# Kernel tuning notes

Hardware: AMD Instinct MI355X
Metric: run time of the kernel (lower is better)

The kernel has to match this reference:

```python
import jax, jax.numpy as jnp
import numpy as np

D = 1024      # model dim
DH = 64       # dim_head
H = 8         # heads
INNER = DH * H
L = 6         # depth
NL = 64       # num_latents
MF = 128      # max_num_frames
FF = 4 * D    # ff_mult * dim
B, T, F, V = 4, 8, 4, 256


def _ln(x, g, b):
    m = x.mean(-1, keepdims=True)
    v = x.var(-1, keepdims=True)
    return (x - m) / jnp.sqrt(v + 1e-5) * g + b


def setup_inputs() -> dict:
    key = jax.random.key(0)
    ks = jax.random.split(key, 8)
    s = 0.02
    x = jax.random.normal(ks[0], (B, T, F, V, D), jnp.float32)
    latents = jax.random.normal(ks[1], (NL, D), jnp.float32)
    frame_embs = jax.random.normal(ks[2], (MF, D), jnp.float32)
    Wq = jax.random.normal(ks[3], (L, D, INNER), jnp.float32) * s
    Wkv = jax.random.normal(ks[4], (L, D, 2 * INNER), jnp.float32) * s
    Wo = jax.random.normal(ks[5], (L, INNER, D), jnp.float32) * s
    W1 = jax.random.normal(ks[6], (L, D, FF), jnp.float32) * s
    W2 = jax.random.normal(ks[7], (L, FF, D), jnp.float32) * s
    ones = jnp.ones((L, D), jnp.float32)
    zeros = jnp.zeros((L, D), jnp.float32)
    return dict(
        x=x, latents=latents, frame_embs=frame_embs,
        g_media=ones, b_media=zeros, g_lat=ones, b_lat=zeros,
        Wq=Wq, Wkv=Wkv, Wo=Wo, g_ff=ones, b_ff=zeros, W1=W1, W2=W2,
        g_out=jnp.ones((D,), jnp.float32), b_out=jnp.zeros((D,), jnp.float32),
    )


def reference(x, latents, frame_embs, g_media, b_media, g_lat, b_lat,
              Wq, Wkv, Wo, g_ff, b_ff, W1, W2, g_out, b_out):
    scale = DH ** -0.5
    # add frame embeddings (indexed by T, as in original code), merge F,v dims
    x = x + frame_embs[:T][None, :, None, None, :]
    x = x.reshape(B, T, F * V, D)
    lat0 = jnp.broadcast_to(latents, (B, T, NL, D))

    def split_heads(a):  # (b, t, n, h*d) -> (b, h, t, n, d)
        return a.reshape(B, T, -1, H, DH).transpose(0, 3, 1, 2, 4)

    def block(lat, p):
        gm, bm, gl, bl, wq, wkv, wo, gf, bf, w1, w2 = p
        xm = _ln(x, gm, bm)
        ln_l = _ln(lat, gl, bl)
        q = (ln_l @ wq) * scale
        kv = jnp.concatenate([xm, ln_l], axis=-2) @ wkv
        k, v = jnp.split(kv, 2, axis=-1)
        q, k, v = split_heads(q), split_heads(k), split_heads(v)
        sim = jnp.einsum('bhtid,bhtjd->bhtij', q, k)
        attn = jax.nn.softmax(sim, axis=-1)
        o = jnp.einsum('bhtij,bhtjd->bhtid', attn, v)
        o = o.transpose(0, 2, 3, 1, 4).reshape(B, T, NL, INNER)
        lat = o @ wo + lat
        ff = jax.nn.gelu(_ln(lat, gf, bf) @ w1, approximate=False) @ w2
        return lat + ff, None

    lat, _ = jax.lax.scan(block, lat0,
                          (g_media, b_media, g_lat, b_lat, Wq, Wkv, Wo,
                           g_ff, b_ff, W1, W2))
    return _ln(lat, g_out, b_out)
```

## Files before the change

### kernel.cpp

```cpp
#include <hip/hip_runtime.h>
#include <math.h>

#define D_      1024
#define DH_     64
#define H_      8
#define INNER_  512
#define L_      6
#define NL_     64
#define FF_     4096
#define B_      4
#define T_      8
#define FV_     1024
#define BT_     32
#define MROWS_  32768
#define NKV_    1088
#define KVROWS_ 34816
#define ZB_     256

typedef __bf16 bf16;
typedef __bf16 bf16x8 __attribute__((ext_vector_type(8)));
typedef __bf16 bf16x4 __attribute__((ext_vector_type(4)));
typedef float  f32x4  __attribute__((ext_vector_type(4)));

#define BARRIER() { asm volatile("" ::: "memory"); __builtin_amdgcn_s_barrier(); asm volatile("" ::: "memory"); }

__device__ __forceinline__ void gload_lds16(const bf16* g, bf16* l) {
    __builtin_amdgcn_global_load_lds(
        (const __attribute__((address_space(1))) unsigned int*)g,
        (__attribute__((address_space(3))) unsigned int*)l, 16, 0, 0);
}

__device__ __forceinline__ float wred_sum(float v) {
#pragma unroll
    for (int o = 32; o > 0; o >>= 1) v += __shfl_xor(v, o, 64);
    return v;
}

__device__ __forceinline__ float gelu_f(float x) {
    return 0.5f * x * (1.0f + erff(x * 0.70710678118654752440f));
}

__global__ __launch_bounds__(256) void xhat_k(const float* __restrict__ x,
                                              const float* __restrict__ fe,
                                              bf16* __restrict__ xhat) {
    __shared__ float red[8];
    int row = blockIdx.x;
    int t = (row >> 10) & 7;
    const float* xr = x + (size_t)row * D_;
    const float* fr_ = fe + (size_t)t * D_;
    int tid = threadIdx.x, c = tid * 4;
    float4 v = *(const float4*)(xr + c);
    float4 f = *(const float4*)(fr_ + c);
    v.x += f.x; v.y += f.y; v.z += f.z; v.w += f.w;
    float s = v.x + v.y + v.z + v.w;
    float ss = v.x * v.x + v.y * v.y + v.z * v.z + v.w * v.w;
    s = wred_sum(s); ss = wred_sum(ss);
    if ((tid & 63) == 0) { red[tid >> 6] = s; red[4 + (tid >> 6)] = ss; }
    __syncthreads();
    s = red[0] + red[1] + red[2] + red[3];
    ss = red[4] + red[5] + red[6] + red[7];
    float mean = s * (1.0f / D_);
    float rstd = rsqrtf(ss * (1.0f / D_) - mean * mean + 1e-5f);
    bf16x4 o;
    o[0] = (bf16)((v.x - mean) * rstd);
    o[1] = (bf16)((v.y - mean) * rstd);
    o[2] = (bf16)((v.z - mean) * rstd);
    o[3] = (bf16)((v.w - mean) * rstd);
    *(bf16x4*)(xhat + (size_t)row * D_ + c) = o;
}

__global__ __launch_bounds__(256) void latinit_k(const float* __restrict__ latents,
                                                 float* __restrict__ lat) {
    int row = blockIdx.x;
    int i = row & 63;
    int c = threadIdx.x * 4;
    float4 v = *(const float4*)(latents + (size_t)i * D_ + c);
    *(float4*)(lat + (size_t)row * D_ + c) = v;
}

template<int OUTF>
__global__ __launch_bounds__(256) void ln_k(const float* __restrict__ in,
                                            const float* __restrict__ g,
                                            const float* __restrict__ b,
                                            void* __restrict__ out) {
    __shared__ float red[8];
    int row = blockIdx.x;
    const float* x = in + (size_t)row * D_;
    int tid = threadIdx.x, c = tid * 4;
    float4 v = *(const float4*)(x + c);
    float s = v.x + v.y + v.z + v.w;
    float ss = v.x * v.x + v.y * v.y + v.z * v.z + v.w * v.w;
    s = wred_sum(s); ss = wred_sum(ss);
    if ((tid & 63) == 0) { red[tid >> 6] = s; red[4 + (tid >> 6)] = ss; }
    __syncthreads();
    s = red[0] + red[1] + red[2] + red[3];
    ss = red[4] + red[5] + red[6] + red[7];
    float mean = s * (1.0f / D_);
    float rstd = rsqrtf(ss * (1.0f / D_) - mean * mean + 1e-5f);
    float4 gv = *(const float4*)(g + c);
    float4 bv = *(const float4*)(b + c);
    float o0 = (v.x - mean) * rstd * gv.x + bv.x;
    float o1 = (v.y - mean) * rstd * gv.y + bv.y;
    float o2 = (v.z - mean) * rstd * gv.z + bv.z;
    float o3 = (v.w - mean) * rstd * gv.w + bv.w;
    if (OUTF) {
        *(float4*)((float*)out + (size_t)row * D_ + c) = make_float4(o0, o1, o2, o3);
    } else {
        bf16x4 o; o[0] = (bf16)o0; o[1] = (bf16)o1; o[2] = (bf16)o2; o[3] = (bf16)o3;
        *(bf16x4*)((bf16*)out + (size_t)row * D_ + c) = o;
    }
}

template<int NP, int OUTF>
__global__ __launch_bounds__(256) void accln_k(float* __restrict__ lat,
                                               const float* __restrict__ p, long long s,
                                               const float* __restrict__ g,
                                               const float* __restrict__ b,
                                               void* __restrict__ out) {
    __shared__ float red[8];
    int row = blockIdx.x;
    int tid = threadIdx.x, c = tid * 4;
    float* lr = lat + (size_t)row * D_;
    float4 a = *(const float4*)(lr + c);
#pragma unroll
    for (int w = 0; w < NP; w++) {
        float4 x = *(const float4*)(p + (size_t)w * s + (size_t)row * D_ + c);
        a.x += x.x; a.y += x.y; a.z += x.z; a.w += x.w;
    }
    if (!OUTF) *(float4*)(lr + c) = a;
    float sm = a.x + a.y + a.z + a.w;
    float ss = a.x * a.x + a.y * a.y + a.z * a.z + a.w * a.w;
    sm = wred_sum(sm); ss = wred_sum(ss);
    if ((tid & 63) == 0) { red[tid >> 6] = sm; red[4 + (tid >> 6)] = ss; }
    __syncthreads();
    sm = red[0] + red[1] + red[2] + red[3];
    ss = red[4] + red[5] + red[6] + red[7];
    float mean = sm * (1.0f / D_);
    float rstd = rsqrtf(ss * (1.0f / D_) - mean * mean + 1e-5f);
    float4 gv = *(const float4*)(g + c);
    float4 bv = *(const float4*)(b + c);
    float o0 = (a.x - mean) * rstd * gv.x + bv.x;
    float o1 = (a.y - mean) * rstd * gv.y + bv.y;
    float o2 = (a.z - mean) * rstd * gv.z + bv.z;
    float o3 = (a.w - mean) * rstd * gv.w + bv.w;
    if (OUTF) {
        *(float4*)((float*)out + (size_t)row * D_ + c) = make_float4(o0, o1, o2, o3);
    } else {
        bf16x4 o; o[0] = (bf16)o0; o[1] = (bf16)o1; o[2] = (bf16)o2; o[3] = (bf16)o3;
        *(bf16x4*)((bf16*)out + (size_t)row * D_ + c) = o;
    }
}

__device__ __forceinline__ void wt_tile(const float* __restrict__ in, int R, int C,
                                        bf16* __restrict__ out, int bx, int by,
                                        const float* __restrict__ sc) {
    __shared__ float t[32][33];
    int c0 = bx * 32, r0 = by * 32;
    int tx = threadIdx.x & 31, ty = threadIdx.x >> 5;
#pragma unroll
    for (int i = 0; i < 4; i++)
        t[ty + i * 8][tx] = in[(size_t)(r0 + ty + i * 8) * C + c0 + tx];
    __syncthreads();
    float scale = sc ? sc[r0 + tx] : 1.0f;
#pragma unroll
    for (int i = 0; i < 4; i++)
        out[(size_t)(c0 + ty + i * 8) * R + r0 + tx] = (bf16)(t[tx][ty + i * 8] * scale);
}

__global__ __launch_bounds__(256) void wprep_k(const float* __restrict__ wq,
                                               const float* __restrict__ wkv,
                                               const float* __restrict__ wo,
                                               const float* __restrict__ w1,
                                               const float* __restrict__ w2,
                                               const float* __restrict__ gm,
                                               bf16* __restrict__ BcatQ,
                                               bf16* __restrict__ BcatKV,
                                               bf16* __restrict__ WkvTg,
                                               bf16* __restrict__ WoT,
                                               bf16* __restrict__ W1T,
                                               bf16* __restrict__ W2T) {
    int id = blockIdx.x;
    if (id < 512)            wt_tile(wq, D_, INNER_, BcatQ, id & 15, id >> 4, nullptr);
    else if (id < 1536)  { int i = id - 512;  wt_tile(wkv, D_, 2 * INNER_, BcatKV, i & 31, i >> 5, nullptr); }
    else if (id < 2560)  { int i = id - 1536; wt_tile(wkv, D_, 2 * INNER_, WkvTg, i & 31, i >> 5, gm); }
    else if (id < 3072)  { int i = id - 2560; wt_tile(wo, INNER_, D_, WoT, i & 31, i >> 5, nullptr); }
    else if (id < 7168)  { int i = id - 3072; wt_tile(w1, D_, FF_, W1T, i & 127, i >> 7, nullptr); }
    else                 { int i = id - 7168; wt_tile(w2, FF_, D_, W2T, i & 31, i >> 5, nullptr); }
}

__global__ __launch_bounds__(256) void bias_k(const float* __restrict__ bm,
                                              const float* __restrict__ wkv,
                                              float* __restrict__ bkv) {
    int n = blockIdx.x * 256 + threadIdx.x;
    float s = 0.0f;
    for (int k = 0; k < D_; k++) s += bm[k] * wkv[(size_t)k * (2 * INNER_) + n];
    bkv[n] = s;
}

__global__ __launch_bounds__(512, 1) void gemm_kv(const bf16* __restrict__ Ag,
                                                  const bf16* __restrict__ Bg,
                                                  bf16* __restrict__ KVb,
                                                  bf16* __restrict__ vt,
                                                  const float* __restrict__ bias) {
    __shared__ bf16 lds[2][32768];
    const int lda = D_, ldb = D_;
    const int tid = threadIdx.x;
    const int w = tid >> 6, lane = tid & 63;
    const int wm = w >> 2, wn = w & 3;
    const size_t m0 = (size_t)blockIdx.x * 256;
    const size_t n0 = (size_t)blockIdx.y * 256;
    const int nt = 16;

    const int p0 = (w * 2) * 64 + lane, p1 = p0 + 64;
    const int sr0 = p0 >> 3, sk0 = ((p0 & 7) ^ (sr0 & 7)) * 8;
    const int sr1 = p1 >> 3, sk1 = ((p1 & 7) ^ (sr1 & 7)) * 8;
    const int scw0 = (w * 2) * 512, scw1 = scw0 + 512;

    auto STAGE = [&](const bf16* g, int ld, size_t row0, int k0, bf16* bufb, int rb) {
        gload_lds16(g + (row0 + sr0) * (size_t)ld + k0 + sk0, bufb + rb + scw0);
        gload_lds16(g + (row0 + sr1) * (size_t)ld + k0 + sk1, bufb + rb + scw1);
    };

    const int fr = lane & 15;
    const int pK0 = (((lane >> 4)) ^ (fr & 7)) * 8;
    const int pK1 = ((4 + (lane >> 4)) ^ (fr & 7)) * 8;
    const size_t aoff = (size_t)(wm * 128 + fr) * 64;
    const size_t boff = 16384 + (size_t)(wn * 64 + fr) * 64;

    f32x4 acc[8][4];
#pragma unroll
    for (int i = 0; i < 8; i++)
#pragma unroll
        for (int j = 0; j < 4; j++)
#pragma unroll
            for (int r = 0; r < 4; r++) acc[i][j][r] = 0.0f;

    STAGE(Bg, ldb, n0,       0, lds[0], 16384);
    STAGE(Bg, ldb, n0 + 128, 0, lds[0], 24576);
    STAGE(Ag, lda, m0,       0, lds[0], 0);
    STAGE(Ag, lda, m0 + 128, 0, lds[0], 8192);
    STAGE(Bg, ldb, n0,       64, lds[1], 16384);
    STAGE(Bg, ldb, n0 + 128, 64, lds[1], 24576);
    STAGE(Ag, lda, m0,       64, lds[1], 0);
    asm volatile("s_waitcnt vmcnt(6)");
    BARRIER();

    for (int t = 0; t < nt; ++t) {
        const bf16* lb = lds[t & 1];
        bf16* lbw = lds[t & 1];
        bf16* lbn = lds[(t + 1) & 1];
        const int kt1 = (t + 1) << 6, kt2 = (t + 2) << 6;
        bf16x8 bfr[4][2];

        {
#pragma unroll
            for (int j = 0; j < 4; j++) {
                bfr[j][0] = *(const bf16x8*)(lb + boff + j * 1024 + pK0);
                bfr[j][1] = *(const bf16x8*)(lb + boff + j * 1024 + pK1);
            }
            bf16x8 a00 = *(const bf16x8*)(lb + aoff + 0 * 1024 + pK0);
            bf16x8 a01 = *(const bf16x8*)(lb + aoff + 0 * 1024 + pK1);
            bf16x8 a10 = *(const bf16x8*)(lb + aoff + 1 * 1024 + pK0);
            bf16x8 a11 = *(const bf16x8*)(lb + aoff + 1 * 1024 + pK1);
            if (t + 1 < nt) STAGE(Ag, lda, m0 + 128, kt1, lbn, 8192);
            BARRIER();
            asm volatile("s_waitcnt lgkmcnt(0)");
            __builtin_amdgcn_s_setprio(1);
#pragma unroll
            for (int j = 0; j < 4; j++) {
                acc[0][j] = __builtin_amdgcn_mfma_f32_16x16x32_bf16(a00, bfr[j][0], acc[0][j], 0, 0, 0);
                acc[0][j] = __builtin_amdgcn_mfma_f32_16x16x32_bf16(a01, bfr[j][1], acc[0][j], 0, 0, 0);
                acc[1][j] = __builtin_amdgcn_mfma_f32_16x16x32_bf16(a10, bfr[j][0], acc[1][j], 0, 0, 0);
                acc[1][j] = __builtin_amdgcn_mfma_f32_16x16x32_bf16(a11, bfr[j][1], acc[1][j], 0, 0, 0);
            }
            __builtin_amdgcn_s_setprio(0);
            BARRIER();
        }
        {
            bf16x8 a00 = *(const bf16x8*)(lb + aoff + 2 * 1024 + pK0);
            bf16x8 a01 = *(const bf16x8*)(lb + aoff + 2 * 1024 + pK1);
            bf16x8 a10 = *(const bf16x8*)(lb + aoff + 3 * 1024 + pK0);
            bf16x8 a11 = *(const bf16x8*)(lb + aoff + 3 * 1024 + pK1);
            if (t + 2 < nt) STAGE(Bg, ldb, n0, kt2, lbw, 16384);
            BARRIER();
            asm volatile("s_waitcnt lgkmcnt(0)");
            __builtin_amdgcn_s_setprio(1);
#pragma unroll
            for (int j = 0; j < 4; j++) {
                acc[2][j] = __builtin_amdgcn_mfma_f32_16x16x32_bf16(a00, bfr[j][0], acc[2][j], 0, 0, 0);
                acc[2][j] = __builtin_amdgcn_mfma_f32_16x16x32_bf16(a01, bfr[j][1], acc[2][j], 0, 0, 0);
                acc[3][j] = __builtin_amdgcn_mfma_f32_16x16x32_bf16(a10, bfr[j][0], acc[3][j], 0, 0, 0);
                acc[3][j] = __builtin_amdgcn_mfma_f32_16x16x32_bf16(a11, bfr[j][1], acc[3][j], 0, 0, 0);
            }
            __builtin_amdgcn_s_setprio(0);
            BARRIER();
        }
        {
            bf16x8 a00 = *(const bf16x8*)(lb + aoff + 4 * 1024 + pK0);
            bf16x8 a01 = *(const bf16x8*)(lb + aoff + 4 * 1024 + pK1);
            bf16x8 a10 = *(const bf16x8*)(lb + aoff + 5 * 1024 + pK0);
            bf16x8 a11 = *(const bf16x8*)(lb + aoff + 5 * 1024 + pK1);
            if (t + 2 < nt) STAGE(Bg, ldb, n0 + 128, kt2, lbw, 24576);
            BARRIER();
            asm volatile("s_waitcnt lgkmcnt(0)");
            __builtin_amdgcn_s_setprio(1);
#pragma unroll
            for (int j = 0; j < 4; j++) {
                acc[4][j] = __builtin_amdgcn_mfma_f32_16x16x32_bf16(a00, bfr[j][0], acc[4][j], 0, 0, 0);
                acc[4][j] = __builtin_amdgcn_mfma_f32_16x16x32_bf16(a01, bfr[j][1], acc[4][j], 0, 0, 0);
                acc[5][j] = __builtin_amdgcn_mfma_f32_16x16x32_bf16(a10, bfr[j][0], acc[5][j], 0, 0, 0);
                acc[5][j] = __builtin_amdgcn_mfma_f32_16x16x32_bf16(a11, bfr[j][1], acc[5][j], 0, 0, 0);
            }
            __builtin_amdgcn_s_setprio(0);
            BARRIER();
        }
        {
            bf16x8 a00 = *(const bf16x8*)(lb + aoff + 6 * 1024 + pK0);
            bf16x8 a01 = *(const bf16x8*)(lb + aoff + 6 * 1024 + pK1);
            bf16x8 a10 = *(const bf16x8*)(lb + aoff + 7 * 1024 + pK0);
            bf16x8 a11 = *(const bf16x8*)(lb + aoff + 7 * 1024 + pK1);
            if (t + 2 < nt) STAGE(Ag, lda, m0, kt2, lbw, 0);
            BARRIER();
            asm volatile("s_waitcnt lgkmcnt(0)");
            __builtin_amdgcn_s_setprio(1);
#pragma unroll
            for (int j = 0; j < 4; j++) {
                acc[6][j] = __builtin_amdgcn_mfma_f32_16x16x32_bf16(a00, bfr[j][0], acc[6][j], 0, 0, 0);
                acc[6][j] = __builtin_amdgcn_mfma_f32_16x16x32_bf16(a01, bfr[j][1], acc[6][j], 0, 0, 0);
                acc[7][j] = __builtin_amdgcn_mfma_f32_16x16x32_bf16(a10, bfr[j][0], acc[7][j], 0, 0, 0);
                acc[7][j] = __builtin_amdgcn_mfma_f32_16x16x32_bf16(a11, bfr[j][1], acc[7][j], 0, 0, 0);
            }
            __builtin_amdgcn_s_setprio(0);
            if (t < nt - 2)       { asm volatile("s_waitcnt vmcnt(6)"); }
            else if (t == nt - 2) { asm volatile("s_waitcnt vmcnt(0)"); }
            BARRIER();
        }
    }

    const int fq = (lane >> 4) * 4;
#pragma unroll
    for (int i = 0; i < 8; i++)
#pragma unroll
        for (int j = 0; j < 4; j++) {
            size_t cb = n0 + wn * 64 + j * 16 + fr;
            float bv = bias[cb];
            size_t mb = m0 + wm * 128 + i * 16 + fq;
            if (cb < 512) {
#pragma unroll
                for (int r = 0; r < 4; r++) {
                    size_t m = mb + r;
                    size_t rb = m + ((m >> 10) << 6);
                    KVb[rb * 512 + cb] = (bf16)(acc[i][j][r] + bv);
                }
            } else {
                int hh = ((int)cb - 512) >> 6, dh = ((int)cb - 512) & 63;
                size_t bt = mb >> 10, jl = mb & 1023;
                bf16x4 v4;
#pragma unroll
                for (int r = 0; r < 4; r++) v4[r] = (bf16)(acc[i][j][r] + bv);
                *(bf16x4*)(vt + ((bt * 8 + hh) * 64 + dh) * (size_t)NKV_ + jl) = v4;
            }
        }
}

template<int MODE, int CMAP>
__global__ __launch_bounds__(256) void gemm128(const bf16* __restrict__ A, int lda,
                                               const bf16* __restrict__ Bw, int ldb,
                                               void* __restrict__ C, int ldc,
                                               int K, float scale,
                                               long long czs, void* __restrict__ C2,
                                               void* __restrict__ C3) {
    __shared__ bf16 As[128 * 32];
    __shared__ bf16 Bs[128 * 32];
    const int tid = threadIdx.x;
    const int wave = tid >> 6;
    const int lane = tid & 63;
    const size_t m0 = (size_t)blockIdx.x * 128;
    const size_t n0 = (size_t)blockIdx.y * 128;
    const int wm = (wave >> 1) * 64;
    const int wn = (wave & 1) * 64;

    const int klen = K / gridDim.z;
    const int koff = blockIdx.z * klen;

    const int r0 = tid >> 2;
    const int c0 = ((tid & 3) ^ ((tid >> 3) & 3)) * 8;
    const bf16* ga0 = A + (m0 + r0) * lda + c0 + koff;
    const bf16* ga1 = A + (m0 + r0 + 64) * lda + c0 + koff;
    const bf16* gb0 = Bw + (n0 + r0) * ldb + c0 + koff;
    const bf16* gb1 = Bw + (n0 + r0 + 64) * ldb + c0 + koff;
    bf16* la0 = As + wave * 512;
    bf16* la1 = As + 2048 + wave * 512;
    bf16* lb0 = Bs + wave * 512;
    bf16* lb1 = Bs + 2048 + wave * 512;

    f32x4 acc[4][4];
#pragma unroll
    for (int i = 0; i < 4; i++)
#pragma unroll
        for (int j = 0; j < 4; j++)
#pragma unroll
            for (int r = 0; r < 4; r++) acc[i][j][r] = 0.0f;

    const int fr = lane & 15;
    const int q = lane >> 4;
    const int sw = (q ^ ((fr >> 1) & 3)) * 8;

    for (int kt = 0; kt < klen; kt += 32) {
        gload_lds16(ga0 + kt, la0);
        gload_lds16(ga1 + kt, la1);
        gload_lds16(gb0 + kt, lb0);
        gload_lds16(gb1 + kt, lb1);
        __syncthreads();
        bf16x8 af[4], bfv[4];
#pragma unroll
        for (int i = 0; i < 4; i++) {
            af[i]  = *(const bf16x8*)(As + (wm + i * 16 + fr) * 32 + sw);
            bfv[i] = *(const bf16x8*)(Bs + (wn + i * 16 + fr) * 32 + sw);
        }
#pragma unroll
        for (int i = 0; i < 4; i++)
#pragma unroll
            for (int j = 0; j < 4; j++)
                acc[i][j] = __builtin_amdgcn_mfma_f32_16x16x32_bf16(af[i], bfv[j], acc[i][j], 0, 0, 0);
        __syncthreads();
    }

    const int fq = (lane >> 4) * 4;
#pragma unroll
    for (int i = 0; i < 4; i++)
#pragma unroll
        for (int j = 0; j < 4; j++) {
            size_t cb = n0 + wn + j * 16 + fr;
            size_t mb = m0 + wm + i * 16 + fq;
            if (CMAP == 3) {
                if (cb < 512) {
#pragma unroll
                    for (int r = 0; r < 4; r++)
                        ((bf16*)C)[(mb + r) * 512 + cb] = (bf16)(acc[i][j][r] * scale);
                } else if (cb < 1024) {
#pragma unroll
                    for (int r = 0; r < 4; r++) {
                        size_t m = mb + r;
                        size_t rb = (m >> 6) * (size_t)NKV_ + 1024 + (m & 63);
                        ((bf16*)C2)[rb * 512 + (cb - 512)] = (bf16)acc[i][j][r];
                    }
                } else {
                    int hh = ((int)cb - 1024) >> 6, dh = ((int)cb - 1024) & 63;
                    size_t bt = mb >> 6, jl = 1024 + (mb & 63);
                    bf16x4 v4;
#pragma unroll
                    for (int r = 0; r < 4; r++) v4[r] = (bf16)acc[i][j][r];
                    *(bf16x4*)((bf16*)C3 + ((bt * 8 + hh) * 64 + dh) * (size_t)NKV_ + jl) = v4;
                }
            } else {
#pragma unroll
                for (int r = 0; r < 4; r++) {
                    float v = acc[i][j][r];
                    if (MODE == 4) {
                        ((float*)C + blockIdx.z * czs)[(mb + r) * ldc + cb] = v;
                    } else {
                        if (MODE == 3) v = gelu_f(v);
                        ((bf16*)C)[(mb + r) * ldc + cb] = (bf16)v;
                    }
                }
            }
        }
}

__global__ __launch_bounds__(256, 2) void attn_k(const bf16* __restrict__ qb,
                                                 const bf16* __restrict__ KVb,
                                                 const bf16* __restrict__ vt,
                                                 bf16* __restrict__ ob) {
    __shared__ float comb[4][64 * 66];
    __shared__ float sc[4][64];
    __shared__ float mw[4][64], lw[4][64];
    const int z = blockIdx.x, bt = z >> 3, h = z & 7;
    const int tid = threadIdx.x, w = tid >> 6, lane = tid & 63;
    const int fr = lane & 15, g = lane >> 4;
    const bf16* Qz = qb + (size_t)(bt * 64) * INNER_ + h * DH_;
    const bf16* Kz = KVb + (size_t)bt * NKV_ * 512 + h * DH_;
    const bf16* Vz = vt + (size_t)z * (DH_ * NKV_);
    bf16* Pw = (bf16*)(&comb[w][0]);

    bf16x8 qf[4][2];
#pragma unroll
    for (int nj = 0; nj < 4; nj++)
#pragma unroll
        for (int ks = 0; ks < 2; ks++)
            qf[nj][ks] = *(const bf16x8*)(Qz + (size_t)(fr + 16 * nj) * INNER_ + g * 8 + ks * 32);

    f32x4 acc_o[4][4];
#pragma unroll
    for (int i = 0; i < 4; i++)
#pragma unroll
        for (int j = 0; j < 4; j++)
#pragma unroll
            for (int r = 0; r < 4; r++) acc_o[i][j][r] = 0.0f;
    float m_reg[4] = {-INFINITY, -INFINITY, -INFINITY, -INFINITY};
    float l_reg[4] = {0.0f, 0.0f, 0.0f, 0.0f};

    const int nch = (w == 0) ? 5 : 4;
    for (int ci = 0; ci < nch; ci++) {
        const int kc0 = (w + ci * 4) * 64;
        f32x4 s[4][4];
#pragma unroll
        for (int i = 0; i < 4; i++)
#pragma unroll
            for (int j = 0; j < 4; j++)
#pragma unroll
                for (int r = 0; r < 4; r++) s[i][j][r] = 0.0f;
#pragma unroll
        for (int ks = 0; ks < 2; ks++) {
            bf16x8 kf[4];
#pragma unroll
            for (int mi = 0; mi < 4; mi++)
                kf[mi] = *(const bf16x8*)(Kz + (size_t)(kc0 + fr + 16 * mi) * 512 + g * 8 + ks * 32);
#pragma unroll
            for (int mi = 0; mi < 4; mi++)
#pragma unroll
                for (int nj = 0; nj < 4; nj++)
                    s[mi][nj] = __builtin_amdgcn_mfma_f32_16x16x32_bf16(kf[mi], qf[nj][ks], s[mi][nj], 0, 0, 0);
        }
        float pmax[4];
#pragma unroll
        for (int nj = 0; nj < 4; nj++) {
            float mx = s[0][nj][0];
#pragma unroll
            for (int mi = 0; mi < 4; mi++)
#pragma unroll
                for (int r = 0; r < 4; r++) mx = fmaxf(mx, s[mi][nj][r]);
            mx = fmaxf(mx, __shfl_xor(mx, 16, 64));
            mx = fmaxf(mx, __shfl_xor(mx, 32, 64));
            pmax[nj] = mx;
        }
        bool grew = (pmax[0] > m_reg[0]) || (pmax[1] > m_reg[1]) ||
                    (pmax[2] > m_reg[2]) || (pmax[3] > m_reg[3]);
        if (__any(grew ? 1 : 0)) {
            float so[4];
#pragma unroll
            for (int nj = 0; nj < 4; nj++) {
                float mn = fmaxf(m_reg[nj], pmax[nj]);
                so[nj] = __expf(m_reg[nj] - mn);
                m_reg[nj] = mn;
                l_reg[nj] *= so[nj];
            }
            if (g == 0) {
#pragma unroll
                for (int nj = 0; nj < 4; nj++) sc[w][fr + 16 * nj] = so[nj];
            }
            asm volatile("s_waitcnt lgkmcnt(0)" ::: "memory");
#pragma unroll
            for (int mi = 0; mi < 4; mi++)
#pragma unroll
                for (int r = 0; r < 4; r++) {
                    float sq = sc[w][16 * mi + 4 * g + r];
#pragma unroll
                    for (int jd = 0; jd < 4; jd++) acc_o[mi][jd][r] *= sq;
                }
        }
        float psum[4] = {0.0f, 0.0f, 0.0f, 0.0f};
#pragma unroll
        for (int mi = 0; mi < 4; mi++)
#pragma unroll
            for (int nj = 0; nj < 4; nj++) {
                bf16x4 pb4;
#pragma unroll
                for (int r = 0; r < 4; r++) {
                    float pv = __expf(s[mi][nj][r] - m_reg[nj]);
                    psum[nj] += pv;
                    pb4[r] = (bf16)pv;
                }
                *(bf16x4*)(Pw + (size_t)(fr + 16 * nj) * 72 + 16 * mi + 4 * g) = pb4;
            }
#pragma unroll
        for (int nj = 0; nj < 4; nj++) {
            float ps = psum[nj];
            ps += __shfl_xor(ps, 16, 64);
            ps += __shfl_xor(ps, 32, 64);
            l_reg[nj] += ps;
        }
        asm volatile("s_waitcnt lgkmcnt(0)" ::: "memory");
#pragma unroll
        for (int ks = 0; ks < 2; ks++) {
            bf16x8 af[4], vf[4];
#pragma unroll
            for (int mi = 0; mi < 4; mi++)
                af[mi] = *(const bf16x8*)(Pw + (size_t)(fr + 16 * mi) * 72 + g * 8 + ks * 32);
#pragma unroll
            for (int jd = 0; jd < 4; jd++)
                vf[jd] = *(const bf16x8*)(Vz + (size_t)(fr + 16 * jd) * NKV_ + kc0 + g * 8 + ks * 32);
#pragma unroll
            for (int mi = 0; mi < 4; mi++)
#pragma unroll
                for (int jd = 0; jd < 4; jd++)
                    acc_o[mi][jd] = __builtin_amdgcn_mfma_f32_16x16x32_bf16(af[mi], vf[jd], acc_o[mi][jd], 0, 0, 0);
        }
    }

    if (g == 0) {
#pragma unroll
        for (int nj = 0; nj < 4; nj++) {
            mw[w][fr + 16 * nj] = m_reg[nj];
            lw[w][fr + 16 * nj] = l_reg[nj];
        }
    }
    asm volatile("s_waitcnt lgkmcnt(0)" ::: "memory");
#pragma unroll
    for (int mi = 0; mi < 4; mi++)
#pragma unroll
        for (int jd = 0; jd < 4; jd++)
#pragma unroll
            for (int r = 0; r < 4; r++)
                comb[w][(16 * mi + 4 * g + r) * 66 + fr + 16 * jd] = acc_o[mi][jd][r];
    __syncthreads();
    {
        int q = tid >> 2, d0 = (tid & 3) * 16;
        float M = fmaxf(fmaxf(mw[0][q], mw[1][q]), fmaxf(mw[2][q], mw[3][q]));
        float al[4], l = 0.0f;
#pragma unroll
        for (int ww = 0; ww < 4; ww++) { al[ww] = __expf(mw[ww][q] - M); l += al[ww] * lw[ww][q]; }
        float inv = 1.0f / l;
        bf16 outv[16];
#pragma unroll
        for (int dd = 0; dd < 16; dd++) {
            float o = 0.0f;
#pragma unroll
            for (int ww = 0; ww < 4; ww++) o += comb[ww][q * 66 + d0 + dd] * al[ww];
            outv[dd] = (bf16)(o * inv);
        }
        bf16* dst = ob + (size_t)(bt * 64 + q) * INNER_ + h * 64 + d0;
        *(bf16x8*)dst = *(bf16x8*)outv;
        *(bf16x8*)(dst + 8) = *(bf16x8*)(outv + 8);
    }
}

extern "C" void kernel_launch(void* const* d_in, const int* in_sizes, int n_in,
                              void* d_out, int out_size, void* d_ws, size_t ws_size,
                              hipStream_t stream) {
    const float* x       = (const float*)d_in[0];
    const float* latents = (const float*)d_in[1];
    const float* fe      = (const float*)d_in[2];
    const float* g_media = (const float*)d_in[3];
    const float* b_media = (const float*)d_in[4];
    const float* g_lat   = (const float*)d_in[5];
    const float* b_lat   = (const float*)d_in[6];
    const float* Wq      = (const float*)d_in[7];
    const float* Wkv     = (const float*)d_in[8];
    const float* Wo      = (const float*)d_in[9];
    const float* g_ff    = (const float*)d_in[10];
    const float* b_ff    = (const float*)d_in[11];
    const float* W1      = (const float*)d_in[12];
    const float* W2      = (const float*)d_in[13];
    const float* g_out   = (const float*)d_in[14];
    const float* b_out   = (const float*)d_in[15];

    char* p = (char*)d_ws;
    auto alloc = [&](size_t bytes) { char* r = p; p += (bytes + 255) & ~(size_t)255; return r; };
    bf16*  xhat = (bf16*)alloc((size_t)MROWS_ * D_ * 2);
    float* lat  = (float*)alloc((size_t)2048 * D_ * 4);
    bf16*  lnl  = (bf16*)alloc((size_t)2048 * D_ * 2);
    bf16*  qb   = (bf16*)alloc((size_t)2048 * INNER_ * 2);
    bf16*  KVb  = (bf16*)alloc((size_t)KVROWS_ * 512 * 2);
    bf16*  vt   = (bf16*)alloc((size_t)ZB_ * DH_ * NKV_ * 2);
    bf16*  ob   = (bf16*)alloc((size_t)2048 * INNER_ * 2);
    bf16*  Bcat = (bf16*)alloc((size_t)1536 * D_ * 2);
    bf16*  WkvTg= (bf16*)alloc((size_t)D_ * D_ * 2);
    bf16*  WoT  = (bf16*)alloc((size_t)D_ * INNER_ * 2);
    bf16*  W1T  = (bf16*)alloc((size_t)FF_ * D_ * 2);
    bf16*  W2T  = (bf16*)alloc((size_t)D_ * FF_ * 2);
    float* bkv  = (float*)alloc(1024 * 4);
    float* ffp  = (float*)alloc((size_t)4 * 2048 * D_ * 4);
    bf16*  ffh  = vt;

    xhat_k<<<MROWS_, 256, 0, stream>>>(x, fe, xhat);
    latinit_k<<<2048, 256, 0, stream>>>(latents, lat);
    ln_k<0><<<2048, 256, 0, stream>>>(lat, g_lat, b_lat, lnl);

    const long long PS = (long long)2048 * D_;

    for (int l = 0; l < L_; l++) {
        const float* gm = g_media + (size_t)l * D_;
        const float* bm = b_media + (size_t)l * D_;
        const float* gf = g_ff + (size_t)l * D_;
        const float* bf_ = b_ff + (size_t)l * D_;
        const float* wq = Wq + (size_t)l * D_ * INNER_;
        const float* wkv = Wkv + (size_t)l * D_ * 2 * INNER_;
        const float* wo = Wo + (size_t)l * INNER_ * D_;
        const float* w1 = W1 + (size_t)l * D_ * FF_;
        const float* w2 = W2 + (size_t)l * FF_ * D_;

        wprep_k<<<11264, 256, 0, stream>>>(wq, wkv, wo, w1, w2, gm,
                                           Bcat, Bcat + (size_t)512 * D_, WkvTg, WoT, W1T, W2T);
        bias_k<<<4, 256, 0, stream>>>(bm, wkv, bkv);

        gemm_kv<<<dim3(128, 4), 512, 0, stream>>>(xhat, WkvTg, KVb, vt, bkv);
        gemm128<0, 3><<<dim3(16, 12), 256, 0, stream>>>(
            lnl, D_, Bcat, D_, qb, 0, D_, 0.125f, 0, KVb, vt);

        attn_k<<<ZB_, 256, 0, stream>>>(qb, KVb, vt, ob);

        gemm128<4, 0><<<dim3(16, 8, 2), 256, 0, stream>>>(
            ob, INNER_, WoT, INNER_, ffp, D_, INNER_, 1.0f, PS, nullptr, nullptr);
        accln_k<2, 0><<<2048, 256, 0, stream>>>(lat, ffp, PS, gf, bf_, lnl);

        gemm128<3, 0><<<dim3(16, 32), 256, 0, stream>>>(
            lnl, D_, W1T, D_, ffh, FF_, D_, 1.0f, 0, nullptr, nullptr);
        gemm128<4, 0><<<dim3(16, 8, 4), 256, 0, stream>>>(
            ffh, FF_, W2T, FF_, ffp, D_, FF_, 1.0f, PS, nullptr, nullptr);
        if (l < L_ - 1) {
            accln_k<4, 0><<<2048, 256, 0, stream>>>(lat, ffp, PS,
                g_lat + (size_t)(l + 1) * D_, b_lat + (size_t)(l + 1) * D_, lnl);
        } else {
            accln_k<4, 1><<<2048, 256, 0, stream>>>(lat, ffp, PS, g_out, b_out, (float*)d_out);
        }
    }
}
```

Baseline: 1.583 ms.

## Software-pipeline GEMM LDS fragment loads, add FF GEMM kernel, fuse bias into wprep

The KV GEMM main loop is restructured so the next A/B fragments are loaded from LDS while the current MFMAs run. The B fragments are double-buffered in registers across K tiles and the wait/barrier points are adjusted. A new 128x256-tile, 512-thread gemm_ff kernel with the same pipelining replaces gemm128 for the two feed-forward GEMMs, with GELU moved into its epilogue. The separate bias kernel is removed and the bias is computed inside the weight-transpose tiles via atomicAdd after a memset, which trades a serial loop for atomics and more register pressure.

```diff
diff --git a/kernel.cpp b/kernel.cpp
--- a/kernel.cpp
+++ b/kernel.cpp
@@ -23,6 +23,7 @@
 typedef float  f32x4  __attribute__((ext_vector_type(4)));
 
 #define BARRIER() { asm volatile("" ::: "memory"); __builtin_amdgcn_s_barrier(); asm volatile("" ::: "memory"); }
+#define ENDPH() { __builtin_amdgcn_sched_barrier(0); asm volatile("s_waitcnt lgkmcnt(0)"); __builtin_amdgcn_sched_barrier(0); BARRIER(); }
 
 __device__ __forceinline__ void gload_lds16(const bf16* g, bf16* l) {
     __builtin_amdgcn_global_load_lds(
@@ -153,7 +154,9 @@
 
 __device__ __forceinline__ void wt_tile(const float* __restrict__ in, int R, int C,
                                         bf16* __restrict__ out, int bx, int by,
-                                        const float* __restrict__ sc) {
+                                        const float* __restrict__ sc,
+                                        const float* __restrict__ bm,
+                                        float* __restrict__ bkv) {
     __shared__ float t[32][33];
     int c0 = bx * 32, r0 = by * 32;
     int tx = threadIdx.x & 31, ty = threadIdx.x >> 5;
@@ -165,6 +168,12 @@
 #pragma unroll
     for (int i = 0; i < 4; i++)
         out[(size_t)(c0 + ty + i * 8) * R + r0 + tx] = (bf16)(t[tx][ty + i * 8] * scale);
+    if (bm && ty == 0) {
+        float s = 0.0f;
+#pragma unroll
+        for (int r = 0; r < 32; r++) s += bm[r0 + r] * t[r][tx];
+        atomicAdd(&bkv[c0 + tx], s);
+    }
 }
 
 __global__ __launch_bounds__(256) void wprep_k(const float* __restrict__ wq,
@@ -173,6 +182,8 @@
                                                const float* __restrict__ w1,
                                                const float* __restrict__ w2,
                                                const float* __restrict__ gm,
+                                               const float* __restrict__ bm,
+                                               float* __restrict__ bkv,
                                                bf16* __restrict__ BcatQ,
                                                bf16* __restrict__ BcatKV,
                                                bf16* __restrict__ WkvTg,
@@ -180,21 +191,12 @@
                                                bf16* __restrict__ W1T,
                                                bf16* __restrict__ W2T) {
     int id = blockIdx.x;
-    if (id < 512)            wt_tile(wq, D_, INNER_, BcatQ, id & 15, id >> 4, nullptr);
-    else if (id < 1536)  { int i = id - 512;  wt_tile(wkv, D_, 2 * INNER_, BcatKV, i & 31, i >> 5, nullptr); }
-    else if (id < 2560)  { int i = id - 1536; wt_tile(wkv, D_, 2 * INNER_, WkvTg, i & 31, i >> 5, gm); }
-    else if (id < 3072)  { int i = id - 2560; wt_tile(wo, INNER_, D_, WoT, i & 31, i >> 5, nullptr); }
-    else if (id < 7168)  { int i = id - 3072; wt_tile(w1, D_, FF_, W1T, i & 127, i >> 7, nullptr); }
-    else                 { int i = id - 7168; wt_tile(w2, FF_, D_, W2T, i & 31, i >> 5, nullptr); }
-}
-
-__global__ __launch_bounds__(256) void bias_k(const float* __restrict__ bm,
-                                              const float* __restrict__ wkv,
-                                              float* __restrict__ bkv) {
-    int n = blockIdx.x * 256 + threadIdx.x;
-    float s = 0.0f;
-    for (int k = 0; k < D_; k++) s += bm[k] * wkv[(size_t)k * (2 * INNER_) + n];
-    bkv[n] = s;
+    if (id < 512)            wt_tile(wq, D_, INNER_, BcatQ, id & 15, id >> 4, nullptr, nullptr, nullptr);
+    else if (id < 1536)  { int i = id - 512;  wt_tile(wkv, D_, 2 * INNER_, BcatKV, i & 31, i >> 5, nullptr, nullptr, nullptr); }
+    else if (id < 2560)  { int i = id - 1536; wt_tile(wkv, D_, 2 * INNER_, WkvTg, i & 31, i >> 5, gm, bm, bkv); }
+    else if (id < 3072)  { int i = id - 2560; wt_tile(wo, INNER_, D_, WoT, i & 31, i >> 5, nullptr, nullptr, nullptr); }
+    else if (id < 7168)  { int i = id - 3072; wt_tile(w1, D_, FF_, W1T, i & 127, i >> 7, nullptr, nullptr, nullptr); }
+    else                 { int i = id - 7168; wt_tile(w2, FF_, D_, W2T, i & 31, i >> 5, nullptr, nullptr, nullptr); }
 }
 
 __global__ __launch_bounds__(512, 1) void gemm_kv(const bf16* __restrict__ Ag,
@@ -235,6 +237,33 @@
 #pragma unroll
             for (int r = 0; r < 4; r++) acc[i][j][r] = 0.0f;
 
+    bf16x8 aX[4], aY[4], bA[4][2], bB[4][2];
+
+    auto LDA2 = [&](const bf16* lb, int i0, bf16x8 (&d)[4]) {
+        d[0] = *(const bf16x8*)(lb + aoff + (size_t)i0 * 1024 + pK0);
+        d[1] = *(const bf16x8*)(lb + aoff + (size_t)i0 * 1024 + pK1);
+        d[2] = *(const bf16x8*)(lb + aoff + (size_t)(i0 + 1) * 1024 + pK0);
+        d[3] = *(const bf16x8*)(lb + aoff + (size_t)(i0 + 1) * 1024 + pK1);
+    };
+    auto LDB8 = [&](const bf16* lb, bf16x8 (&bb)[4][2]) {
+#pragma unroll
+        for (int j = 0; j < 4; j++) {
+            bb[j][0] = *(const bf16x8*)(lb + boff + j * 1024 + pK0);
+            bb[j][1] = *(const bf16x8*)(lb + boff + j * 1024 + pK1);
+        }
+    };
+    auto MM2 = [&](int i0, bf16x8 (&a)[4], bf16x8 (&bb)[4][2]) {
+        __builtin_amdgcn_s_setprio(1);
+#pragma unroll
+        for (int j = 0; j < 4; j++) {
+            acc[i0][j]     = __builtin_amdgcn_mfma_f32_16x16x32_bf16(a[0], bb[j][0], acc[i0][j], 0, 0, 0);
+            acc[i0][j]     = __builtin_amdgcn_mfma_f32_16x16x32_bf16(a[1], bb[j][1], acc[i0][j], 0, 0, 0);
+            acc[i0 + 1][j] = __builtin_amdgcn_mfma_f32_16x16x32_bf16(a[2], bb[j][0], acc[i0 + 1][j], 0, 0, 0);
+            acc[i0 + 1][j] = __builtin_amdgcn_mfma_f32_16x16x32_bf16(a[3], bb[j][1], acc[i0 + 1][j], 0, 0, 0);
+        }
+        __builtin_amdgcn_s_setprio(0);
+    };
+
     STAGE(Bg, ldb, n0,       0, lds[0], 16384);
     STAGE(Bg, ldb, n0 + 128, 0, lds[0], 24576);
     STAGE(Ag, lda, m0,       0, lds[0], 0);
@@ -244,97 +273,37 @@
     STAGE(Ag, lda, m0,       64, lds[1], 0);
     asm volatile("s_waitcnt vmcnt(6)");
     BARRIER();
-
-    for (int t = 0; t < nt; ++t) {
-        const bf16* lb = lds[t & 1];
-        bf16* lbw = lds[t & 1];
-        bf16* lbn = lds[(t + 1) & 1];
-        const int kt1 = (t + 1) << 6, kt2 = (t + 2) << 6;
-        bf16x8 bfr[4][2];
-
-        {
-#pragma unroll
-            for (int j = 0; j < 4; j++) {
-                bfr[j][0] = *(const bf16x8*)(lb + boff + j * 1024 + pK0);
-                bfr[j][1] = *(const bf16x8*)(lb + boff + j * 1024 + pK1);
-            }
-            bf16x8 a00 = *(const bf16x8*)(lb + aoff + 0 * 1024 + pK0);
-            bf16x8 a01 = *(const bf16x8*)(lb + aoff + 0 * 1024 + pK1);
-            bf16x8 a10 = *(const bf16x8*)(lb + aoff + 1 * 1024 + pK0);
-            bf16x8 a11 = *(const bf16x8*)(lb + aoff + 1 * 1024 + pK1);
-            if (t + 1 < nt) STAGE(Ag, lda, m0 + 128, kt1, lbn, 8192);
-            BARRIER();
-            asm volatile("s_waitcnt lgkmcnt(0)");
-            __builtin_amdgcn_s_setprio(1);
-#pragma unroll
-            for (int j = 0; j < 4; j++) {
-                acc[0][j] = __builtin_amdgcn_mfma_f32_16x16x32_bf16(a00, bfr[j][0], acc[0][j], 0, 0, 0);
-                acc[0][j] = __builtin_amdgcn_mfma_f32_16x16x32_bf16(a01, bfr[j][1], acc[0][j], 0, 0, 0);
-                acc[1][j] = __builtin_amdgcn_mfma_f32_16x16x32_bf16(a10, bfr[j][0], acc[1][j], 0, 0, 0);
-                acc[1][j] = __builtin_amdgcn_mfma_f32_16x16x32_bf16(a11, bfr[j][1], acc[1][j], 0, 0, 0);
-            }
-            __builtin_amdgcn_s_setprio(0);
-            BARRIER();
-        }
-        {
-            bf16x8 a00 = *(const bf16x8*)(lb + aoff + 2 * 1024 + pK0);
-            bf16x8 a01 = *(const bf16x8*)(lb + aoff + 2 * 1024 + pK1);
-            bf16x8 a10 = *(const bf16x8*)(lb + aoff + 3 * 1024 + pK0);
-            bf16x8 a11 = *(const bf16x8*)(lb + aoff + 3 * 1024 + pK1);
-            if (t + 2 < nt) STAGE(Bg, ldb, n0, kt2, lbw, 16384);
-            BARRIER();
-            asm volatile("s_waitcnt lgkmcnt(0)");
-            __builtin_amdgcn_s_setprio(1);
-#pragma unroll
-            for (int j = 0; j < 4; j++) {
-                acc[2][j] = __builtin_amdgcn_mfma_f32_16x16x32_bf16(a00, bfr[j][0], acc[2][j], 0, 0, 0);
-                acc[2][j] = __builtin_amdgcn_mfma_f32_16x16x32_bf16(a01, bfr[j][1], acc[2][j], 0, 0, 0);
-                acc[3][j] = __builtin_amdgcn_mfma_f32_16x16x32_bf16(a10, bfr[j][0], acc[3][j], 0, 0, 0);
-                acc[3][j] = __builtin_amdgcn_mfma_f32_16x16x32_bf16(a11, bfr[j][1], acc[3][j], 0, 0, 0);
-            }
-            __builtin_amdgcn_s_setprio(0);
-            BARRIER();
-        }
-        {
-            bf16x8 a00 = *(const bf16x8*)(lb + aoff + 4 * 1024 + pK0);
-            bf16x8 a01 = *(const bf16x8*)(lb + aoff + 4 * 1024 + pK1);
-            bf16x8 a10 = *(const bf16x8*)(lb + aoff + 5 * 1024 + pK0);
-            bf16x8 a11 = *(const bf16x8*)(lb + aoff + 5 * 1024 + pK1);
-            if (t + 2 < nt) STAGE(Bg, ldb, n0 + 128, kt2, lbw, 24576);
-            BARRIER();
-            asm volatile("s_waitcnt lgkmcnt(0)");
-            __builtin_amdgcn_s_setprio(1);
-#pragma unroll
-            for (int j = 0; j < 4; j++) {
-                acc[4][j] = __builtin_amdgcn_mfma_f32_16x16x32_bf16(a00, bfr[j][0], acc[4][j], 0, 0, 0);
-                acc[4][j] = __builtin_amdgcn_mfma_f32_16x16x32_bf16(a01, bfr[j][1], acc[4][j], 0, 0, 0);
-                acc[5][j] = __builtin_amdgcn_mfma_f32_16x16x32_bf16(a10, bfr[j][0], acc[5][j], 0, 0, 0);
-                acc[5][j] = __builtin_amdgcn_mfma_f32_16x16x32_bf16(a11, bfr[j][1], acc[5][j], 0, 0, 0);
-            }
-            __builtin_amdgcn_s_setprio(0);
-            BARRIER();
-        }
-        {
-            bf16x8 a00 = *(const bf16x8*)(lb + aoff + 6 * 1024 + pK0);
-            bf16x8 a01 = *(const bf16x8*)(lb + aoff + 6 * 1024 + pK1);
-            bf16x8 a10 = *(const bf16x8*)(lb + aoff + 7 * 1024 + pK0);
-            bf16x8 a11 = *(const bf16x8*)(lb + aoff + 7 * 1024 + pK1);
-            if (t + 2 < nt) STAGE(Ag, lda, m0, kt2, lbw, 0);
-            BARRIER();
-            asm volatile("s_waitcnt lgkmcnt(0)");
-            __builtin_amdgcn_s_setprio(1);
-#pragma unroll
-            for (int j = 0; j < 4; j++) {
-                acc[6][j] = __builtin_amdgcn_mfma_f32_16x16x32_bf16(a00, bfr[j][0], acc[6][j], 0, 0, 0);
-                acc[6][j] = __builtin_amdgcn_mfma_f32_16x16x32_bf16(a01, bfr[j][1], acc[6][j], 0, 0, 0);
-                acc[7][j] = __builtin_amdgcn_mfma_f32_16x16x32_bf16(a10, bfr[j][0], acc[7][j], 0, 0, 0);
-                acc[7][j] = __builtin_amdgcn_mfma_f32_16x16x32_bf16(a11, bfr[j][1], acc[7][j], 0, 0, 0);
-            }
-            __builtin_amdgcn_s_setprio(0);
-            if (t < nt - 2)       { asm volatile("s_waitcnt vmcnt(6)"); }
-            else if (t == nt - 2) { asm volatile("s_waitcnt vmcnt(0)"); }
-            BARRIER();
-        }
+    LDB8(lds[0], bA);
+    LDA2(lds[0], 0, aX);
+
+    auto tile4 = [&](const bf16* lb, bf16* lbn, bf16x8 (&BU)[4][2], bf16x8 (&BL)[4][2], int t) {
+        bf16* lbw = (bf16*)lb;
+        LDA2(lb, 2, aY);
+        if (t + 1 < nt) STAGE(Ag, lda, m0 + 128, (t + 1) << 6, lbn, 8192);
+        MM2(0, aX, BU);
+        ENDPH();
+        LDA2(lb, 4, aX);
+        if (t + 2 < nt) STAGE(Bg, ldb, n0, (t + 2) << 6, lbw, 16384);
+        MM2(2, aY, BU);
+        ENDPH();
+        LDA2(lb, 6, aY);
+        if (t + 2 < nt) STAGE(Bg, ldb, n0 + 128, (t + 2) << 6, lbw, 24576);
+        MM2(4, aX, BU);
+        __builtin_amdgcn_sched_barrier(0);
+        asm volatile("s_waitcnt lgkmcnt(0)");
+        __builtin_amdgcn_sched_barrier(0);
+        if (t < nt - 2)       { asm volatile("s_waitcnt vmcnt(4)"); }
+        else if (t == nt - 2) { asm volatile("s_waitcnt vmcnt(0)"); }
+        BARRIER();
+        if (t + 1 < nt) { LDB8(lbn, BL); LDA2(lbn, 0, aX); }
+        if (t + 2 < nt) STAGE(Ag, lda, m0, (t + 2) << 6, lbw, 0);
+        MM2(6, aY, BU);
+        ENDPH();
+    };
+
+    for (int t = 0; t < nt; t += 2) {
+        tile4(lds[0], lds[1], bA, bB, t);
+        tile4(lds[1], lds[0], bB, bA, t + 1);
     }
 
     const int fq = (lane >> 4) * 4;
@@ -359,6 +328,126 @@
 #pragma unroll
                 for (int r = 0; r < 4; r++) v4[r] = (bf16)(acc[i][j][r] + bv);
                 *(bf16x4*)(vt + ((bt * 8 + hh) * 64 + dh) * (size_t)NKV_ + jl) = v4;
+            }
+        }
+}
+
+template<int MODE>
+__global__ __launch_bounds__(512, 1) void gemm_ff(const bf16* __restrict__ Ag, int lda,
+                                                  const bf16* __restrict__ Bg, int ldb,
+                                                  void* __restrict__ C, int ldc,
+                                                  int K, long long czs) {
+    __shared__ bf16 lds[2][24576];
+    const int tid = threadIdx.x;
+    const int w = tid >> 6, lane = tid & 63;
+    const int wm = w >> 2, wn = w & 3;
+    const size_t m0 = (size_t)blockIdx.x * 128;
+    const size_t n0 = (size_t)blockIdx.y * 256;
+    const int klen = K / gridDim.z;
+    const int koff = blockIdx.z * klen;
+    const int nt = klen >> 6;
+
+    const int p0 = (w * 2) * 64 + lane, p1 = p0 + 64;
+    const int sr0 = p0 >> 3, sk0 = ((p0 & 7) ^ (sr0 & 7)) * 8;
+    const int sr1 = p1 >> 3, sk1 = ((p1 & 7) ^ (sr1 & 7)) * 8;
+    const int scw0 = (w * 2) * 512, scw1 = scw0 + 512;
+
+    auto STAGE = [&](const bf16* g, int ld, size_t row0, int k0, bf16* bufb, int rb) {
+        gload_lds16(g + (row0 + sr0) * (size_t)ld + k0 + sk0, bufb + rb + scw0);
+        gload_lds16(g + (row0 + sr1) * (size_t)ld + k0 + sk1, bufb + rb + scw1);
+    };
+
+    const int fr = lane & 15;
+    const int pK0 = (((lane >> 4)) ^ (fr & 7)) * 8;
+    const int pK1 = ((4 + (lane >> 4)) ^ (fr & 7)) * 8;
+    const size_t aoff = (size_t)(wm * 64 + fr) * 64;
+    const size_t boff = 8192 + (size_t)(wn * 64 + fr) * 64;
+
+    f32x4 acc[4][4];
+#pragma unroll
+    for (int i = 0; i < 4; i++)
+#pragma unroll
+        for (int j = 0; j < 4; j++)
+#pragma unroll
+            for (int r = 0; r < 4; r++) acc[i][j][r] = 0.0f;
+
+    bf16x8 aX[2], aY[2], bA[4][2], bB[4][2];
+
+    auto LDA1 = [&](const bf16* lb, int i0, bf16x8 (&d)[2]) {
+        d[0] = *(const bf16x8*)(lb + aoff + (size_t)i0 * 1024 + pK0);
+        d[1] = *(const bf16x8*)(lb + aoff + (size_t)i0 * 1024 + pK1);
+    };
+    auto LDB8 = [&](const bf16* lb, bf16x8 (&bb)[4][2]) {
+#pragma unroll
+        for (int j = 0; j < 4; j++) {
+            bb[j][0] = *(const bf16x8*)(lb + boff + j * 1024 + pK0);
+            bb[j][1] = *(const bf16x8*)(lb + boff + j * 1024 + pK1);
+        }
+    };
+    auto MM1 = [&](int i0, bf16x8 (&a)[2], bf16x8 (&bb)[4][2]) {
+        __builtin_amdgcn_s_setprio(1);
+#pragma unroll
+        for (int j = 0; j < 4; j++) {
+            acc[i0][j] = __builtin_amdgcn_mfma_f32_16x16x32_bf16(a[0], bb[j][0], acc[i0][j], 0, 0, 0);
+            acc[i0][j] = __builtin_amdgcn_mfma_f32_16x16x32_bf16(a[1], bb[j][1], acc[i0][j], 0, 0, 0);
+        }
+        __builtin_amdgcn_s_setprio(0);
+    };
+
+    STAGE(Ag, lda, m0,       koff,      lds[0], 0);
+    STAGE(Bg, ldb, n0,       koff,      lds[0], 8192);
+    STAGE(Bg, ldb, n0 + 128, koff,      lds[0], 16384);
+    STAGE(Bg, ldb, n0,       koff + 64, lds[1], 8192);
+    STAGE(Bg, ldb, n0 + 128, koff + 64, lds[1], 16384);
+    asm volatile("s_waitcnt vmcnt(4)");
+    BARRIER();
+    LDB8(lds[0], bA);
+    LDA1(lds[0], 0, aX);
+
+    auto tile4 = [&](const bf16* lb, bf16* lbn, bf16x8 (&BU)[4][2], bf16x8 (&BL)[4][2], int t) {
+        bf16* lbw = (bf16*)lb;
+        LDA1(lb, 1, aY);
+        if (t + 1 < nt) STAGE(Ag, lda, m0, koff + ((t + 1) << 6), lbn, 0);
+        MM1(0, aX, BU);
+        ENDPH();
+        LDA1(lb, 2, aX);
+        if (t + 2 < nt) STAGE(Bg, ldb, n0, koff + ((t + 2) << 6), lbw, 8192);
+        MM1(1, aY, BU);
+        ENDPH();
+        LDA1(lb, 3, aY);
+        if (t + 2 < nt) STAGE(Bg, ldb, n0 + 128, koff + ((t + 2) << 6), lbw, 16384);
+        MM1(2, aX, BU);
+        __builtin_amdgcn_sched_barrier(0);
+        asm volatile("s_waitcnt lgkmcnt(0)");
+        __builtin_amdgcn_sched_barrier(0);
+        if (t < nt - 2)       { asm volatile("s_waitcnt vmcnt(4)"); }
+        else if (t == nt - 2) { asm volatile("s_waitcnt vmcnt(0)"); }
+        BARRIER();
+        if (t + 1 < nt) { LDB8(lbn, BL); LDA1(lbn, 0, aX); }
+        MM1(3, aY, BU);
+        ENDPH();
+    };
+
+    for (int t = 0; t < nt; t += 2) {
+        tile4(lds[0], lds[1], bA, bB, t);
+        tile4(lds[1], lds[0], bB, bA, t + 1);
+    }
+
+    const int fq = (lane >> 4) * 4;
+#pragma unroll
+    for (int i = 0; i < 4; i++)
+#pragma unroll
+        for (int j = 0; j < 4; j++) {
+            size_t cb = n0 + wn * 64 + j * 16 + fr;
+            size_t mb = m0 + wm * 64 + i * 16 + fq;
+#pragma unroll
+            for (int r = 0; r < 4; r++) {
+                float v = acc[i][j][r];
+                if (MODE == 4) {
+                    ((float*)C + blockIdx.z * czs)[(mb + r) * (size_t)ldc + cb] = v;
+                } else {
+                    ((bf16*)C)[(mb + r) * (size_t)ldc + cb] = (bf16)gelu_f(v);
+                }
             }
         }
 }
@@ -460,7 +549,6 @@
                     if (MODE == 4) {
                         ((float*)C + blockIdx.z * czs)[(mb + r) * ldc + cb] = v;
                     } else {
-                        if (MODE == 3) v = gelu_f(v);
                         ((bf16*)C)[(mb + r) * ldc + cb] = (bf16)v;
                     }
                 }
@@ -690,9 +778,9 @@
         const float* w1 = W1 + (size_t)l * D_ * FF_;
         const float* w2 = W2 + (size_t)l * FF_ * D_;
 
-        wprep_k<<<11264, 256, 0, stream>>>(wq, wkv, wo, w1, w2, gm,
+        hipMemsetAsync(bkv, 0, 1024 * 4, stream);
+        wprep_k<<<11264, 256, 0, stream>>>(wq, wkv, wo, w1, w2, gm, bm, bkv,
                                            Bcat, Bcat + (size_t)512 * D_, WkvTg, WoT, W1T, W2T);
-        bias_k<<<4, 256, 0, stream>>>(bm, wkv, bkv);
 
         gemm_kv<<<dim3(128, 4), 512, 0, stream>>>(xhat, WkvTg, KVb, vt, bkv);
         gemm128<0, 3><<<dim3(16, 12), 256, 0, stream>>>(
@@ -704,10 +792,10 @@
             ob, INNER_, WoT, INNER_, ffp, D_, INNER_, 1.0f, PS, nullptr, nullptr);
         accln_k<2, 0><<<2048, 256, 0, stream>>>(lat, ffp, PS, gf, bf_, lnl);
 
-        gemm128<3, 0><<<dim3(16, 32), 256, 0, stream>>>(
-            lnl, D_, W1T, D_, ffh, FF_, D_, 1.0f, 0, nullptr, nullptr);
-        gemm128<4, 0><<<dim3(16, 8, 4), 256, 0, stream>>>(
-            ffh, FF_, W2T, FF_, ffp, D_, FF_, 1.0f, PS, nullptr, nullptr);
+        gemm_ff<3><<<dim3(16, 16), 512, 0, stream>>>(
+            lnl, D_, W1T, D_, ffh, FF_, D_, 0);
+        gemm_ff<4><<<dim3(16, 4, 4), 512, 0, stream>>>(
+            ffh, FF_, W2T, FF_, ffp, D_, FF_, PS);
         if (l < L_ - 1) {
             accln_k<4, 0><<<2048, 256, 0, stream>>>(lat, ffp, PS,
                 g_lat + (size_t)(l + 1) * D_, b_lat + (size_t)(l + 1) * D_, lnl);
```

Result: faster. 1.324 ms (-16.3%).
